# Kernel optimization log

Measured on AMD Instinct MI355X. Metric: run time of the kernel, lower is better.

## Reference

```python
import jax, jax.numpy as jnp
import numpy as np

NUM_NODES = 1024
K = 16384
G = 128

def setup_inputs() -> dict:
    key = jax.random.key(0)
    k1, k2, k3 = jax.random.split(key, 3)
    x = jax.random.normal(k1, (G, NUM_NODES, 64), dtype=jnp.float32)
    # original draws fresh xavier-uniform embeddings inside forward; we
    # materialize equivalent random embeddings here (only ordering matters).
    emb_s = jax.random.normal(k2, (G, NUM_NODES, 1), dtype=jnp.float32)
    emb_t = jax.random.normal(k3, (G, 1, NUM_NODES), dtype=jnp.float32)
    return {"x": x, "emb_s": emb_s, "emb_t": emb_t}

def reference(x, emb_s, emb_t):
    num_graphs = x.shape[0]
    n = NUM_NODES
    # rank-1 outer product adjacency: [G, N, N]
    adj = emb_s * emb_t  # broadcast (G,N,1)*(G,1,N)
    # mask diagonal with -inf
    diag = jnp.eye(n, dtype=bool)
    adj = jnp.where(diag[None, :, :], -jnp.inf, adj)
    # global top-k over flattened N*N per graph
    adj_flat = adj.reshape(num_graphs, n * n)
    _, indices = jax.lax.top_k(adj_flat, K)  # [G, K]
    # scatter ones at selected positions
    out_flat = jnp.zeros((num_graphs, n * n), dtype=adj.dtype)
    rows = jnp.arange(num_graphs)[:, None]
    out_flat = out_flat.at[rows, indices].set(1.0)
    return out_flat.reshape(num_graphs, n, n)
```

## Files before the change

### kernel.cpp

```cpp
#include <hip/hip_runtime.h>
#include <stdint.h>

#define NNODES 1024
#define NGRAPH 128
#define TOPK   16384
#define EQCAP  4096

__device__ __forceinline__ uint32_t fkey(float x) {
    uint32_t u = __float_as_uint(x);
    return (u & 0x80000000u) ? ~u : (u | 0x80000000u);
}

__global__ __launch_bounds__(NNODES)
void select_kernel(const float* __restrict__ s, const float* __restrict__ t,
                   uint32_t* __restrict__ Tout, uint32_t* __restrict__ Rout,
                   uint32_t* __restrict__ eqCntG, uint32_t* __restrict__ eqIdxG) {
    const int g = blockIdx.x, i = threadIdx.x;
    __shared__ float    torig[NNODES];
    __shared__ uint32_t skey[NNODES];
    __shared__ uint16_t sidx[NNODES];
    __shared__ float    tvs[NNODES];
    __shared__ uint32_t wsum[16];
    __shared__ uint32_t sLo, sHi, sDir, sEqCnt;
    __shared__ uint32_t sEqList[EQCAP];

    const float tv_i = t[g * NNODES + i];
    torig[i] = tv_i;
    skey[i]  = fkey(tv_i);
    sidx[i]  = (uint16_t)i;
    if (i == 0) { sLo = 0u; sHi = 0xFFFFFFFFu; sEqCnt = 0u; }

    for (int k = 2; k <= NNODES; k <<= 1) {
        for (int j = k >> 1; j > 0; j >>= 1) {
            __syncthreads();
            int partner = i ^ j;
            if (partner > i) {
                bool asc = ((i & k) == 0);
                uint32_t a = skey[i], b = skey[partner];
                if ((a > b) == asc) {
                    skey[i] = b; skey[partner] = a;
                    uint16_t ia = sidx[i]; sidx[i] = sidx[partner]; sidx[partner] = ia;
                }
            }
        }
    }
    __syncthreads();
    tvs[i] = torig[sidx[i]];

    const float sv = s[g * NNODES + i];
    const bool sneg = (__float_as_uint(sv) >> 31) != 0;
    const uint32_t kdiag = fkey(sv * tv_i);
    __syncthreads();

    auto srchRange = [&](uint32_t cand, int lo, int hi) -> int {
        while (lo < hi) {
            int mid = (lo + hi) >> 1;
            bool pred = fkey(sv * tvs[mid]) > cand;
            bool goLeft = sneg ? !pred : pred;
            if (goLeft) hi = mid; else lo = mid + 1;
        }
        return lo;
    };

    int rlo = 0, rhi = NNODES;

    for (int it = 0; it < 33; ++it) {
        const uint32_t lo = sLo, hi = sHi;
        const uint32_t mid = lo + ((hi - lo) >> 1);
        const int b = srchRange(mid, rlo, rhi);
        uint32_t c = sneg ? (uint32_t)b : (uint32_t)(NNODES - b);
        if (kdiag > mid) c--;
        uint32_t r = c;
        for (int off = 32; off; off >>= 1) r += __shfl_down(r, off);
        if ((i & 63) == 0) wsum[i >> 6] = r;
        __syncthreads();
        if (i == 0 && lo < hi) {
            uint32_t tot = 0;
            for (int w = 0; w < 16; ++w) tot += wsum[w];
            if (tot < TOPK) { sHi = mid; sDir = 0u; }
            else            { sLo = mid + 1; sDir = 1u; }
        }
        __syncthreads();
        if (lo < hi) {
            if (sDir == 0u) { if (!sneg) rhi = b; else rlo = b; }
            else            { if (!sneg) rlo = b; else rhi = b; }
        }
    }
    const uint32_t T = sLo;

    {
        const int b = srchRange(T, rlo, rhi);
        uint32_t c = sneg ? (uint32_t)b : (uint32_t)(NNODES - b);
        if (kdiag > T) c--;
        uint32_t r = c;
        for (int off = 32; off; off >>= 1) r += __shfl_down(r, off);
        if ((i & 63) == 0) wsum[i >> 6] = r;
        __syncthreads();
        if (i == 0) {
            uint32_t tot = 0;
            for (int w = 0; w < 16; ++w) tot += wsum[w];
            Tout[g] = T; Rout[g] = TOPK - tot;
        }
    }
    __syncthreads();

    auto bound = [&](bool ge) -> int {
        int lo = 0, hi = NNODES;
        while (lo < hi) {
            int mid = (lo + hi) >> 1;
            uint32_t k = fkey(sv * tvs[mid]);
            bool pred = ge ? (k >= T) : (k > T);
            bool goLeft = sneg ? !pred : pred;
            if (goLeft) hi = mid; else lo = mid + 1;
        }
        return lo;
    };
    int e0, e1;
    if (!sneg) { e0 = bound(true);  e1 = bound(false); }
    else       { e0 = bound(false); e1 = bound(true);  }
    for (int p = e0; p < e1; ++p) {
        uint32_t j = sidx[p];
        if ((int)j == i) continue;
        uint32_t slot = atomicAdd(&sEqCnt, 1u);
        if (slot < EQCAP) sEqList[slot] = (uint32_t)(i * NNODES) + j;
    }
    __syncthreads();
    uint32_t E = sEqCnt; if (E > EQCAP) E = EQCAP;
    if (i == 0) eqCntG[g] = E;
    for (uint32_t p = i; p < E; p += NNODES) eqIdxG[g * EQCAP + p] = sEqList[p];
}

__global__ __launch_bounds__(256)
void write_kernel(const float* __restrict__ s, const float* __restrict__ t,
                  const uint32_t* __restrict__ Tin, float* __restrict__ out) {
    const int b = blockIdx.x;
    const int g = b >> 10, i = b & 1023;
    const uint32_t T = Tin[g];
    const float sv = s[(size_t)g * NNODES + i];
    const float4 tv = ((const float4*)(t + (size_t)g * NNODES))[threadIdx.x];
    const int j0 = threadIdx.x * 4;
    float4 r;
    r.x = (fkey(sv * tv.x) > T && (j0 + 0) != i) ? 1.0f : 0.0f;
    r.y = (fkey(sv * tv.y) > T && (j0 + 1) != i) ? 1.0f : 0.0f;
    r.z = (fkey(sv * tv.z) > T && (j0 + 2) != i) ? 1.0f : 0.0f;
    r.w = (fkey(sv * tv.w) > T && (j0 + 3) != i) ? 1.0f : 0.0f;
    ((float4*)(out + (size_t)g * NNODES * NNODES + (size_t)i * NNODES))[threadIdx.x] = r;
}

__global__ __launch_bounds__(256)
void scatter_kernel(const uint32_t* __restrict__ eqCnt, const uint32_t* __restrict__ eqIdx,
                    const uint32_t* __restrict__ Rin, float* __restrict__ out) {
    const int g = blockIdx.x;
    uint32_t E = eqCnt[g];
    const uint32_t R = Rin[g];
    __shared__ uint32_t se[EQCAP];
    for (uint32_t p = threadIdx.x; p < E; p += blockDim.x) se[p] = eqIdx[g * EQCAP + p];
    __syncthreads();
    for (uint32_t p = threadIdx.x; p < E; p += blockDim.x) {
        uint32_t v = se[p], rank = 0;
        for (uint32_t q = 0; q < E; ++q) rank += (se[q] < v) ? 1u : 0u;
        if (rank < R) out[(size_t)g * NNODES * NNODES + v] = 1.0f;
    }
}

extern "C" void kernel_launch(void* const* d_in, const int* in_sizes, int n_in,
                              void* d_out, int out_size, void* d_ws, size_t ws_size,
                              hipStream_t stream) {
    const float* s = (const float*)d_in[1];
    const float* t = (const float*)d_in[2];
    float* out = (float*)d_out;

    char* ws = (char*)d_ws;
    uint32_t* Tbuf  = (uint32_t*)ws; ws += (size_t)NGRAPH * 4;
    uint32_t* Rbuf  = (uint32_t*)ws; ws += (size_t)NGRAPH * 4;
    uint32_t* eqCnt = (uint32_t*)ws; ws += (size_t)NGRAPH * 4;
    uint32_t* eqIdx = (uint32_t*)ws; ws += (size_t)NGRAPH * EQCAP * 4;

    select_kernel<<<NGRAPH, NNODES, 0, stream>>>(s, t, Tbuf, Rbuf, eqCnt, eqIdx);
    write_kernel<<<NGRAPH * NNODES, 256, 0, stream>>>(s, t, Tbuf, out);
    scatter_kernel<<<NGRAPH, 256, 0, stream>>>(eqCnt, eqIdx, Rbuf, out);
}
```

Before: 141.8 us.

## Register bitonic sort with wave shuffles, barrier-light threshold search, multi-row write blocks

The select kernel now sorts packed key/index pairs held in registers. It uses wave shuffles for small strides and double-buffered shared memory for large ones, which removes most block barriers. The threshold binary search has every thread reduce the per-wave sums itself, so the single-thread update and one barrier per iteration go away. The final recount is dropped by reusing the count saved at the last upper-bound update. The write kernel now handles 16 rows per block instead of one, cutting block count and launch overhead at the cost of less parallelism per block.

```diff
diff --git a/kernel.cpp b/kernel.cpp
--- a/kernel.cpp
+++ b/kernel.cpp
@@ -5,10 +5,15 @@
 #define NGRAPH 128
 #define TOPK   16384
 #define EQCAP  4096
+#define WROWS  16
 
 __device__ __forceinline__ uint32_t fkey(float x) {
     uint32_t u = __float_as_uint(x);
     return (u & 0x80000000u) ? ~u : (u | 0x80000000u);
+}
+__device__ __forceinline__ float inv_fkey(uint32_t k) {
+    uint32_t u = (k & 0x80000000u) ? (k & 0x7FFFFFFFu) : ~k;
+    return __uint_as_float(u);
 }
 
 __global__ __launch_bounds__(NNODES)
@@ -16,104 +21,87 @@
                    uint32_t* __restrict__ Tout, uint32_t* __restrict__ Rout,
                    uint32_t* __restrict__ eqCntG, uint32_t* __restrict__ eqIdxG) {
     const int g = blockIdx.x, i = threadIdx.x;
-    __shared__ float    torig[NNODES];
-    __shared__ uint32_t skey[NNODES];
+    __shared__ uint64_t xbuf[2][NNODES];
+    __shared__ float    tvs[NNODES];
     __shared__ uint16_t sidx[NNODES];
-    __shared__ float    tvs[NNODES];
-    __shared__ uint32_t wsum[16];
-    __shared__ uint32_t sLo, sHi, sDir, sEqCnt;
+    __shared__ uint32_t wsum[2][16];
+    __shared__ uint32_t sEqCnt;
     __shared__ uint32_t sEqList[EQCAP];
 
     const float tv_i = t[g * NNODES + i];
-    torig[i] = tv_i;
-    skey[i]  = fkey(tv_i);
-    sidx[i]  = (uint16_t)i;
-    if (i == 0) { sLo = 0u; sHi = 0xFFFFFFFFu; sEqCnt = 0u; }
+    uint64_t e = ((uint64_t)fkey(tv_i) << 16) | (uint32_t)i;
+    if (i == 0) sEqCnt = 0u;
 
+    int pb = 0;
     for (int k = 2; k <= NNODES; k <<= 1) {
         for (int j = k >> 1; j > 0; j >>= 1) {
-            __syncthreads();
-            int partner = i ^ j;
-            if (partner > i) {
-                bool asc = ((i & k) == 0);
-                uint32_t a = skey[i], b = skey[partner];
-                if ((a > b) == asc) {
-                    skey[i] = b; skey[partner] = a;
-                    uint16_t ia = sidx[i]; sidx[i] = sidx[partner]; sidx[partner] = ia;
-                }
+            uint64_t pe;
+            if (j >= 64) {
+                xbuf[pb][i] = e;
+                __syncthreads();
+                pe = xbuf[pb][i ^ j];
+                pb ^= 1;
+            } else {
+                pe = (uint64_t)__shfl_xor((unsigned long long)e, j, 64);
             }
+            bool keepSmall = (((i & j) == 0) == ((i & k) == 0));
+            e = (keepSmall == (pe < e)) ? pe : e;
         }
     }
-    __syncthreads();
-    tvs[i] = torig[sidx[i]];
+    tvs[i]  = inv_fkey((uint32_t)(e >> 16));
+    sidx[i] = (uint16_t)(e & 0xFFFFu);
 
     const float sv = s[g * NNODES + i];
     const bool sneg = (__float_as_uint(sv) >> 31) != 0;
     const uint32_t kdiag = fkey(sv * tv_i);
     __syncthreads();
 
-    auto srchRange = [&](uint32_t cand, int lo, int hi) -> int {
-        while (lo < hi) {
-            int mid = (lo + hi) >> 1;
+    auto srchRange = [&](uint32_t cand, int lo_, int hi_) -> int {
+        while (lo_ < hi_) {
+            int mid = (lo_ + hi_) >> 1;
             bool pred = fkey(sv * tvs[mid]) > cand;
             bool goLeft = sneg ? !pred : pred;
-            if (goLeft) hi = mid; else lo = mid + 1;
+            if (goLeft) hi_ = mid; else lo_ = mid + 1;
         }
-        return lo;
+        return lo_;
     };
 
+    uint32_t lo = 0u, hi = 0xFFFFFFFFu;
+    uint32_t cntHi = 0u;
     int rlo = 0, rhi = NNODES;
-
     for (int it = 0; it < 33; ++it) {
-        const uint32_t lo = sLo, hi = sHi;
         const uint32_t mid = lo + ((hi - lo) >> 1);
         const int b = srchRange(mid, rlo, rhi);
         uint32_t c = sneg ? (uint32_t)b : (uint32_t)(NNODES - b);
         if (kdiag > mid) c--;
         uint32_t r = c;
         for (int off = 32; off; off >>= 1) r += __shfl_down(r, off);
-        if ((i & 63) == 0) wsum[i >> 6] = r;
+        if ((i & 63) == 0) wsum[pb][i >> 6] = r;
         __syncthreads();
-        if (i == 0 && lo < hi) {
-            uint32_t tot = 0;
-            for (int w = 0; w < 16; ++w) tot += wsum[w];
-            if (tot < TOPK) { sHi = mid; sDir = 0u; }
-            else            { sLo = mid + 1; sDir = 1u; }
-        }
-        __syncthreads();
+        uint32_t tot = 0;
+        #pragma unroll
+        for (int w = 0; w < 16; ++w) tot += wsum[pb][w];
+        pb ^= 1;
         if (lo < hi) {
-            if (sDir == 0u) { if (!sneg) rhi = b; else rlo = b; }
-            else            { if (!sneg) rlo = b; else rhi = b; }
+            if (tot < TOPK) { hi = mid; cntHi = tot;
+                              if (!sneg) rhi = b; else rlo = b; }
+            else            { lo = mid + 1;
+                              if (!sneg) rlo = b; else rhi = b; }
         }
     }
-    const uint32_t T = sLo;
-
-    {
-        const int b = srchRange(T, rlo, rhi);
-        uint32_t c = sneg ? (uint32_t)b : (uint32_t)(NNODES - b);
-        if (kdiag > T) c--;
-        uint32_t r = c;
-        for (int off = 32; off; off >>= 1) r += __shfl_down(r, off);
-        if ((i & 63) == 0) wsum[i >> 6] = r;
-        __syncthreads();
-        if (i == 0) {
-            uint32_t tot = 0;
-            for (int w = 0; w < 16; ++w) tot += wsum[w];
-            Tout[g] = T; Rout[g] = TOPK - tot;
-        }
-    }
-    __syncthreads();
+    const uint32_t T = lo;
+    if (i == 0) { Tout[g] = T; Rout[g] = TOPK - cntHi; }
 
     auto bound = [&](bool ge) -> int {
-        int lo = 0, hi = NNODES;
-        while (lo < hi) {
-            int mid = (lo + hi) >> 1;
+        int lo_ = 0, hi_ = NNODES;
+        while (lo_ < hi_) {
+            int mid = (lo_ + hi_) >> 1;
             uint32_t k = fkey(sv * tvs[mid]);
             bool pred = ge ? (k >= T) : (k > T);
             bool goLeft = sneg ? !pred : pred;
-            if (goLeft) hi = mid; else lo = mid + 1;
+            if (goLeft) hi_ = mid; else lo_ = mid + 1;
         }
-        return lo;
+        return lo_;
     };
     int e0, e1;
     if (!sneg) { e0 = bound(true);  e1 = bound(false); }
@@ -133,18 +121,24 @@
 __global__ __launch_bounds__(256)
 void write_kernel(const float* __restrict__ s, const float* __restrict__ t,
                   const uint32_t* __restrict__ Tin, float* __restrict__ out) {
-    const int b = blockIdx.x;
-    const int g = b >> 10, i = b & 1023;
+    const int b  = blockIdx.x;
+    const int g  = b >> 6;
+    const int i0 = (b & 63) * WROWS;
     const uint32_t T = Tin[g];
-    const float sv = s[(size_t)g * NNODES + i];
     const float4 tv = ((const float4*)(t + (size_t)g * NNODES))[threadIdx.x];
     const int j0 = threadIdx.x * 4;
-    float4 r;
-    r.x = (fkey(sv * tv.x) > T && (j0 + 0) != i) ? 1.0f : 0.0f;
-    r.y = (fkey(sv * tv.y) > T && (j0 + 1) != i) ? 1.0f : 0.0f;
-    r.z = (fkey(sv * tv.z) > T && (j0 + 2) != i) ? 1.0f : 0.0f;
-    r.w = (fkey(sv * tv.w) > T && (j0 + 3) != i) ? 1.0f : 0.0f;
-    ((float4*)(out + (size_t)g * NNODES * NNODES + (size_t)i * NNODES))[threadIdx.x] = r;
+    float4* orow = (float4*)(out + (size_t)g * NNODES * NNODES + (size_t)i0 * NNODES);
+    #pragma unroll
+    for (int r = 0; r < WROWS; ++r) {
+        const int i = i0 + r;
+        const float sv = s[(size_t)g * NNODES + i];
+        float4 o;
+        o.x = (fkey(sv * tv.x) > T && (j0 + 0) != i) ? 1.0f : 0.0f;
+        o.y = (fkey(sv * tv.y) > T && (j0 + 1) != i) ? 1.0f : 0.0f;
+        o.z = (fkey(sv * tv.z) > T && (j0 + 2) != i) ? 1.0f : 0.0f;
+        o.w = (fkey(sv * tv.w) > T && (j0 + 3) != i) ? 1.0f : 0.0f;
+        orow[(size_t)r * (NNODES / 4) + threadIdx.x] = o;
+    }
 }
 
 __global__ __launch_bounds__(256)
@@ -177,6 +171,6 @@
     uint32_t* eqIdx = (uint32_t*)ws; ws += (size_t)NGRAPH * EQCAP * 4;
 
     select_kernel<<<NGRAPH, NNODES, 0, stream>>>(s, t, Tbuf, Rbuf, eqCnt, eqIdx);
-    write_kernel<<<NGRAPH * NNODES, 256, 0, stream>>>(s, t, Tbuf, out);
+    write_kernel<<<NGRAPH * (NNODES / WROWS), 256, 0, stream>>>(s, t, Tbuf, out);
     scatter_kernel<<<NGRAPH, 256, 0, stream>>>(eqCnt, eqIdx, Rbuf, out);
 }
```

New measurement: 151.7 us. 1.07x slower.

## Use 4-way threshold search with packed 64-bit counts and fewer barriers

Applied to the files above, without the earlier changes.

Replaces the 33-step binary search for the top-k threshold key with an 18-step quaternary search. Each step evaluates three candidates per thread and packs the three counts into one 64-bit value. The counts are reduced with wave shuffles plus a shared atomic into a rotating triple buffer, so each step needs one barrier instead of two and the final count pass is dropped. Every thread keeps lo/hi in registers and updates them identically. The aim is to cut the serial barrier-bound critical path of select_kernel, at the cost of more binary-search work per iteration.

```diff
diff --git a/kernel.cpp b/kernel.cpp
--- a/kernel.cpp
+++ b/kernel.cpp
@@ -20,15 +20,16 @@
     __shared__ uint32_t skey[NNODES];
     __shared__ uint16_t sidx[NNODES];
     __shared__ float    tvs[NNODES];
-    __shared__ uint32_t wsum[16];
-    __shared__ uint32_t sLo, sHi, sDir, sEqCnt;
+    __shared__ uint64_t sTot[3];
+    __shared__ uint32_t sEqCnt;
     __shared__ uint32_t sEqList[EQCAP];
 
     const float tv_i = t[g * NNODES + i];
     torig[i] = tv_i;
     skey[i]  = fkey(tv_i);
     sidx[i]  = (uint16_t)i;
-    if (i == 0) { sLo = 0u; sHi = 0xFFFFFFFFu; sEqCnt = 0u; }
+    if (i == 0) sEqCnt = 0u;
+    if (i < 3)  sTot[i] = 0ull;
 
     for (int k = 2; k <= NNODES; k <<= 1) {
         for (int j = k >> 1; j > 0; j >>= 1) {
@@ -52,68 +53,77 @@
     const uint32_t kdiag = fkey(sv * tv_i);
     __syncthreads();
 
-    auto srchRange = [&](uint32_t cand, int lo, int hi) -> int {
-        while (lo < hi) {
-            int mid = (lo + hi) >> 1;
+    auto srchRange = [&](uint32_t cand, int lo_, int hi_) -> int {
+        while (lo_ < hi_) {
+            int mid = (lo_ + hi_) >> 1;
             bool pred = fkey(sv * tvs[mid]) > cand;
             bool goLeft = sneg ? !pred : pred;
-            if (goLeft) hi = mid; else lo = mid + 1;
+            if (goLeft) hi_ = mid; else lo_ = mid + 1;
         }
-        return lo;
+        return lo_;
     };
 
+    uint32_t lo = 0u, hi = 0xFFFFFFFFu;
+    uint32_t cntHi = 0u;
     int rlo = 0, rhi = NNODES;
-
-    for (int it = 0; it < 33; ++it) {
-        const uint32_t lo = sLo, hi = sHi;
-        const uint32_t mid = lo + ((hi - lo) >> 1);
-        const int b = srchRange(mid, rlo, rhi);
-        uint32_t c = sneg ? (uint32_t)b : (uint32_t)(NNODES - b);
-        if (kdiag > mid) c--;
-        uint32_t r = c;
-        for (int off = 32; off; off >>= 1) r += __shfl_down(r, off);
-        if ((i & 63) == 0) wsum[i >> 6] = r;
+    for (int it = 0; it < 18; ++it) {
+        const uint32_t range = hi - lo;
+        const uint32_t c0 = lo + (uint32_t)(((uint64_t)range * 1) >> 2);
+        const uint32_t c1 = lo + (uint32_t)(((uint64_t)range * 2) >> 2);
+        const uint32_t c2 = lo + (uint32_t)(((uint64_t)range * 3) >> 2);
+        int b0, b1, b2;
+        if (!sneg) {
+            b0 = srchRange(c0, rlo, rhi);
+            b1 = srchRange(c1, b0,  rhi);
+            b2 = srchRange(c2, b1,  rhi);
+        } else {
+            b0 = srchRange(c0, rlo, rhi);
+            b1 = srchRange(c1, rlo, b0);
+            b2 = srchRange(c2, rlo, b1);
+        }
+        uint32_t n0 = sneg ? (uint32_t)b0 : (uint32_t)(NNODES - b0);
+        uint32_t n1 = sneg ? (uint32_t)b1 : (uint32_t)(NNODES - b1);
+        uint32_t n2 = sneg ? (uint32_t)b2 : (uint32_t)(NNODES - b2);
+        if (kdiag > c0) n0--;
+        if (kdiag > c1) n1--;
+        if (kdiag > c2) n2--;
+        uint64_t r = (uint64_t)n0 | ((uint64_t)n1 << 21) | ((uint64_t)n2 << 42);
+        for (int off = 32; off; off >>= 1)
+            r += (uint64_t)__shfl_down((unsigned long long)r, off);
+        if ((i & 63) == 0)
+            atomicAdd((unsigned long long*)&sTot[it % 3], (unsigned long long)r);
+        if (i == 0) sTot[(it + 1) % 3] = 0ull;
         __syncthreads();
-        if (i == 0 && lo < hi) {
-            uint32_t tot = 0;
-            for (int w = 0; w < 16; ++w) tot += wsum[w];
-            if (tot < TOPK) { sHi = mid; sDir = 0u; }
-            else            { sLo = mid + 1; sDir = 1u; }
-        }
-        __syncthreads();
+        const uint64_t tot = sTot[it % 3];
+        const uint32_t t0 = (uint32_t)(tot & 0x1FFFFFu);
+        const uint32_t t1 = (uint32_t)((tot >> 21) & 0x1FFFFFu);
+        const uint32_t t2 = (uint32_t)((tot >> 42) & 0x1FFFFFu);
         if (lo < hi) {
-            if (sDir == 0u) { if (!sneg) rhi = b; else rlo = b; }
-            else            { if (!sneg) rlo = b; else rhi = b; }
+            if (t0 < TOPK)      { hi = c0; cntHi = t0;
+                                  if (!sneg) rhi = b0; else rlo = b0; }
+            else if (t1 < TOPK) { lo = c0 + 1; hi = c1; cntHi = t1;
+                                  if (!sneg) { rlo = b0; rhi = b1; }
+                                  else       { rlo = b1; rhi = b0; } }
+            else if (t2 < TOPK) { lo = c1 + 1; hi = c2; cntHi = t2;
+                                  if (!sneg) { rlo = b1; rhi = b2; }
+                                  else       { rlo = b2; rhi = b1; } }
+            else                { lo = c2 + 1;
+                                  if (!sneg) rlo = b2; else rhi = b2; }
         }
     }
-    const uint32_t T = sLo;
-
-    {
-        const int b = srchRange(T, rlo, rhi);
-        uint32_t c = sneg ? (uint32_t)b : (uint32_t)(NNODES - b);
-        if (kdiag > T) c--;
-        uint32_t r = c;
-        for (int off = 32; off; off >>= 1) r += __shfl_down(r, off);
-        if ((i & 63) == 0) wsum[i >> 6] = r;
-        __syncthreads();
-        if (i == 0) {
-            uint32_t tot = 0;
-            for (int w = 0; w < 16; ++w) tot += wsum[w];
-            Tout[g] = T; Rout[g] = TOPK - tot;
-        }
-    }
-    __syncthreads();
+    const uint32_t T = lo;
+    if (i == 0) { Tout[g] = T; Rout[g] = TOPK - cntHi; }
 
     auto bound = [&](bool ge) -> int {
-        int lo = 0, hi = NNODES;
-        while (lo < hi) {
-            int mid = (lo + hi) >> 1;
+        int lo_ = 0, hi_ = NNODES;
+        while (lo_ < hi_) {
+            int mid = (lo_ + hi_) >> 1;
             uint32_t k = fkey(sv * tvs[mid]);
             bool pred = ge ? (k >= T) : (k > T);
             bool goLeft = sneg ? !pred : pred;
-            if (goLeft) hi = mid; else lo = mid + 1;
+            if (goLeft) hi_ = mid; else lo_ = mid + 1;
         }
-        return lo;
+        return lo_;
     };
     int e0, e1;
     if (!sneg) { e0 = bound(true);  e1 = bound(false); }
```

After: 150.2 us. 1.06x slower.
